# Optimization experiments

Measured on AMD Instinct MI355X. Metric: run time of the kernel, lower is better.

Reference implementation:

```python
import jax, jax.numpy as jnp
import numpy as np

N = 131072   # atoms
D = 384      # aev dim
E = 4        # experts (elements)
H1, H2, H3 = 256, 192, 160


def setup_inputs() -> dict:
    key = jax.random.key(0)
    ks = jax.random.split(key, 12)
    s = 0.05
    inp = {
        "aev": jax.random.normal(ks[0], (N, D), dtype=jnp.float32),
        "index": jax.random.randint(ks[1], (N,), 0, E),
        # stacked per-expert MLP weights [E, in, out]
        "W1": jax.random.normal(ks[2], (E, D, H1), dtype=jnp.float32) * s,
        "b1": jax.random.normal(ks[3], (E, H1), dtype=jnp.float32) * s,
        "W2": jax.random.normal(ks[4], (E, H1, H2), dtype=jnp.float32) * s,
        "b2": jax.random.normal(ks[5], (E, H2), dtype=jnp.float32) * s,
        "W3": jax.random.normal(ks[6], (E, H2, H3), dtype=jnp.float32) * s,
        "b3": jax.random.normal(ks[7], (E, H3), dtype=jnp.float32) * s,
        "W4": jax.random.normal(ks[8], (E, H3, 1), dtype=jnp.float32) * s,
        "b4": jax.random.normal(ks[9], (E, 1), dtype=jnp.float32) * s,
        "alphas": jnp.ones((E,), dtype=jnp.float32),
        "shifts": jnp.array([-0.5, -37.8, -54.5, -75.0], dtype=jnp.float32),
    }
    return inp


def reference(aev, index, W1, b1, W2, b2, W3, b3, W4, b4, alphas, shifts):
    # Run all E expert MLPs densely on all atoms, then select per-atom by index.
    # Same math per selected expert as torch masked dispatch/combine.
    h = jax.nn.celu(jnp.einsum('nd,edh->enh', aev, W1) + b1[:, None, :])
    h = jax.nn.celu(jnp.einsum('enh,ehk->enk', h, W2) + b2[:, None, :])
    h = jax.nn.celu(jnp.einsum('enk,ekm->enm', h, W3) + b3[:, None, :])
    y = (jnp.einsum('enm,emo->eno', h, W4) + b4[:, None, :])[..., 0]  # [E, N]
    y = y * alphas[:, None] + shifts[:, None]                         # shifted nets
    out = jnp.take_along_axis(y, index[None, :], axis=0)[0]           # [N]
    return out
```

## Files before the change

kernel.cpp:

```cpp
#include <hip/hip_runtime.h>
#include <hip/hip_bf16.h>

#define NATOMS 131072
#define DIM    384
#define NE     4
#define H1N    256
#define H2N    192
#define H3N    160
#define BM     64
#define NTH    256
#define NTILES (NATOMS/BM + NE)

typedef __attribute__((ext_vector_type(8))) short bf16x8;
typedef __attribute__((ext_vector_type(4))) float f32x4;
typedef __attribute__((ext_vector_type(4))) int   i32x4;
typedef __attribute__((ext_vector_type(2))) int   i32x2;

#define WS_META   0
#define WS_TABLE  64
#define WS_PERM   (WS_TABLE + NTILES*16)
#define WS_WT1    ((WS_PERM + NATOMS*4 + 255) & ~255)
#define SZ_WT1    (NE*H1N*DIM*2)
#define WS_WT2    (WS_WT1 + SZ_WT1)
#define SZ_WT2    (NE*H2N*H1N*2)
#define WS_WT3    (WS_WT2 + SZ_WT2)
#define SZ_WT3    (NE*H3N*H2N*2)

#define L_ROWS 0
#define L_H1   256
#define L_H2   (L_H1 + BM*528)
#define LDS_TOTAL (L_H2 + BM*400)

static __device__ __forceinline__ unsigned short f2bf(float f) {
  union { __hip_bfloat16 h; unsigned short u; } v;
  v.h = __float2bfloat16(f);
  return v.u;
}
static __device__ __forceinline__ unsigned pack2(float a, float b) {
  union { __hip_bfloat162 h2; unsigned u; } v;
  v.h2 = __float22bfloat162_rn(make_float2(a, b));
  return v.u;
}
static __device__ __forceinline__ float celu1(float x) {
  return x > 0.f ? x : (__expf(x) - 1.f);
}
static __device__ __forceinline__ bf16x8 cvt8(f32x4 a, f32x4 b) {
  union { bf16x8 v; unsigned u[4]; } r;
  r.u[0] = pack2(a.x, a.y); r.u[1] = pack2(a.z, a.w);
  r.u[2] = pack2(b.x, b.y); r.u[3] = pack2(b.z, b.w);
  return r.v;
}

__global__ void k_zero(int* meta) {
  if (threadIdx.x < 16) meta[threadIdx.x] = 0;
}

__global__ void k_wprep(const float* __restrict__ W1, const float* __restrict__ W2,
                        const float* __restrict__ W3,
                        unsigned short* __restrict__ wt1,
                        unsigned short* __restrict__ wt2,
                        unsigned short* __restrict__ wt3) {
  __shared__ float t[32][33];
  int b = blockIdx.x;
  const float* W; unsigned short* wt; int K, NN, ntiles, idx;
  if (b < 384)      { W = W1; wt = wt1; K = 384; NN = 256; ntiles = 8; idx = b; }
  else if (b < 576) { W = W2; wt = wt2; K = 256; NN = 192; ntiles = 6; idx = b - 384; }
  else              { W = W3; wt = wt3; K = 192; NN = 160; ntiles = 5; idx = b - 576; }
  int per_e = (K / 32) * ntiles;
  int e  = idx / per_e;
  int r  = idx % per_e;
  int kt = r / ntiles, nt = r % ntiles;

  int row = threadIdx.x >> 3, c4 = (threadIdx.x & 7) * 4;
  float4 v = *(const float4*)(W + ((size_t)(e * K + kt * 32 + row) * NN + nt * 32 + c4));
  t[row][c4 + 0] = v.x; t[row][c4 + 1] = v.y;
  t[row][c4 + 2] = v.z; t[row][c4 + 3] = v.w;
  __syncthreads();

  int n = threadIdx.x >> 3, k4 = (threadIdx.x & 7) * 4;
  unsigned short o[4];
  o[0] = f2bf(t[k4 + 0][n]); o[1] = f2bf(t[k4 + 1][n]);
  o[2] = f2bf(t[k4 + 2][n]); o[3] = f2bf(t[k4 + 3][n]);
  i32x2 p; p.x = (int)(o[0] | ((unsigned)o[1] << 16));
  p.y = (int)(o[2] | ((unsigned)o[3] << 16));
  *(i32x2*)(wt + ((size_t)(e * (K / 32) + kt) * NN + nt * 32 + n) * 32 + k4) = p;
}

__global__ void k_hist(const int* __restrict__ index, int* __restrict__ meta) {
  __shared__ int h[NE];
  int t = threadIdx.x;
  if (t < NE) h[t] = 0;
  __syncthreads();
  int b0 = blockIdx.x * 1024;
  #pragma unroll
  for (int j = 0; j < 4; ++j) atomicAdd(&h[index[b0 + t + j*256]], 1);
  __syncthreads();
  if (t < NE) atomicAdd(&meta[t], h[t]);
}

__global__ void k_plan(int* __restrict__ meta, i32x4* __restrict__ table) {
  __shared__ int off[NE + 1], nt[NE + 1];
  if (threadIdx.x == 0) {
    int o = 0, t = 0;
    for (int e = 0; e < NE; ++e) {
      off[e] = o; nt[e] = t;
      o += meta[e];
      t += (meta[e] + BM - 1) / BM;
      meta[4 + e] = off[e];
    }
    off[NE] = o; nt[NE] = t;
  }
  __syncthreads();
  for (int i = threadIdx.x; i < NTILES; i += blockDim.x) {
    i32x4 v = {0, 0, 0, 0};
    for (int e = 0; e < NE; ++e) {
      if (i >= nt[e] && i < nt[e + 1]) {
        int local = i - nt[e];
        int cnt = off[e + 1] - off[e];
        int rem = cnt - local * BM;
        v.x = e; v.y = off[e] + local * BM; v.z = rem < BM ? rem : BM;
      }
    }
    table[i] = v;
  }
}

__global__ void k_scatter(const int* __restrict__ index, int* __restrict__ meta,
                          int* __restrict__ perm) {
  __shared__ int h[NE], base[NE];
  int t = threadIdx.x;
  if (t < NE) h[t] = 0;
  __syncthreads();
  int b0 = blockIdx.x * 1024;
  int eIdx[4];
  #pragma unroll
  for (int j = 0; j < 4; ++j) {
    eIdx[j] = index[b0 + t + j*256];
    atomicAdd(&h[eIdx[j]], 1);
  }
  __syncthreads();
  if (t < NE) { base[t] = atomicAdd(&meta[4 + t], h[t]); h[t] = 0; }
  __syncthreads();
  #pragma unroll
  for (int j = 0; j < 4; ++j) {
    int e = eIdx[j];
    int slot = atomicAdd(&h[e], 1);
    perm[base[e] + slot] = b0 + t + j*256;
  }
}

__launch_bounds__(NTH, 2)
__global__ void k_mlp(const float* __restrict__ aev,
                      const unsigned short* __restrict__ wt1,
                      const unsigned short* __restrict__ wt2,
                      const unsigned short* __restrict__ wt3,
                      const float* __restrict__ b1g,
                      const float* __restrict__ b2g,
                      const float* __restrict__ b3g,
                      const float* __restrict__ w4g,
                      const float* __restrict__ b4g,
                      const float* __restrict__ alpg,
                      const float* __restrict__ shfg,
                      const int* __restrict__ perm,
                      const i32x4* __restrict__ table,
                      float* __restrict__ out)
{
  extern __shared__ char smem[];
  int* ldsRows = (int*)(smem + L_ROWS);

  i32x4 tt = table[blockIdx.x];
  const int e = tt.x, start = tt.y, len = tt.z;
  if (len == 0) return;

  const int tid = threadIdx.x;
  const int l   = tid & 63;
  const int w   = tid >> 6;
  const int l15 = l & 15;
  const int lg  = l >> 4;
  const int l4o = lg * 16;
  const int r4  = lg * 4;
  const int wn  = w & 1;
  const int wm  = w >> 1;

  if (tid < BM) ldsRows[tid] = (tid < len) ? perm[start + tid] : -1;

  const float* xp[2];
  #pragma unroll
  for (int mi = 0; mi < 2; ++mi) {
    int row = wm * 32 + mi * 16 + l15;
    int ar = (row < len) ? perm[start + row] : 0;
    xp[mi] = aev + (size_t)ar * DIM + lg * 8;
  }

  {
    f32x4 acc[8][2];
    #pragma unroll
    for (int a = 0; a < 8; ++a)
      #pragma unroll
      for (int b = 0; b < 2; ++b)
        acc[a][b] = f32x4{0.f, 0.f, 0.f, 0.f};

    const unsigned short* w1base =
        wt1 + (size_t)e * (12 * 256 * 32) + (wn * 128 + l15) * 32 + lg * 8;

    bf16x8 af[2][8];
    f32x4  xr[3][2][2];
    #pragma unroll
    for (int s = 0; s < 3; ++s)
      #pragma unroll
      for (int mi = 0; mi < 2; ++mi) {
        xr[s][mi][0] = *(const f32x4*)(xp[mi] + s * 32);
        xr[s][mi][1] = *(const f32x4*)(xp[mi] + s * 32 + 4);
      }
    #pragma unroll
    for (int ni = 0; ni < 8; ++ni)
      af[0][ni] = *(const bf16x8*)(w1base + ni * 512);

    #pragma unroll
    for (int kk = 0; kk < 12; ++kk) {
      const int cb = kk & 1, xb = kk % 3;
      if (kk + 1 < 12) {
        #pragma unroll
        for (int ni = 0; ni < 8; ++ni)
          af[cb ^ 1][ni] = *(const bf16x8*)(w1base + (kk + 1) * 8192 + ni * 512);
      }
      bf16x8 bx[2];
      #pragma unroll
      for (int mi = 0; mi < 2; ++mi) {
        bx[mi] = cvt8(xr[xb][mi][0], xr[xb][mi][1]);
        if (kk + 3 < 12) {
          xr[xb][mi][0] = *(const f32x4*)(xp[mi] + (kk + 3) * 32);
          xr[xb][mi][1] = *(const f32x4*)(xp[mi] + (kk + 3) * 32 + 4);
        }
      }
      #pragma unroll
      for (int ni = 0; ni < 8; ++ni)
        #pragma unroll
        for (int mi = 0; mi < 2; ++mi)
          acc[ni][mi] = __builtin_amdgcn_mfma_f32_16x16x32_bf16(
              af[cb][ni], bx[mi], acc[ni][mi], 0, 0, 0);
    }
    #pragma unroll
    for (int ni = 0; ni < 8; ++ni) {
      const int nb = wn * 128 + ni * 16 + r4;
      float4 bias = *(const float4*)(b1g + e * H1N + nb);
      #pragma unroll
      for (int mi = 0; mi < 2; ++mi) {
        const int m = wm * 32 + mi * 16 + l15;
        f32x4 v = acc[ni][mi];
        i32x2 p;
        p.x = (int)pack2(celu1(v.x + bias.x), celu1(v.y + bias.y));
        p.y = (int)pack2(celu1(v.z + bias.z), celu1(v.w + bias.w));
        *(i32x2*)(smem + L_H1 + m * 528 + nb * 2) = p;
      }
    }
  }
  __syncthreads();

  {
    f32x4 acc[6][2];
    #pragma unroll
    for (int a = 0; a < 6; ++a)
      #pragma unroll
      for (int b = 0; b < 2; ++b)
        acc[a][b] = f32x4{0.f, 0.f, 0.f, 0.f};

    const unsigned short* w2base =
        wt2 + (size_t)e * (8 * 192 * 32) + (wn * 96 + l15) * 32 + lg * 8;
    const int hbase = L_H1 + (wm * 32 + l15) * 528 + l4o;

    bf16x8 af[2][6];
    #pragma unroll
    for (int ni = 0; ni < 6; ++ni)
      af[0][ni] = *(const bf16x8*)(w2base + ni * 512);

    #pragma unroll
    for (int kk = 0; kk < 8; ++kk) {
      const int cb = kk & 1;
      if (kk + 1 < 8) {
        #pragma unroll
        for (int ni = 0; ni < 6; ++ni)
          af[cb ^ 1][ni] = *(const bf16x8*)(w2base + (kk + 1) * 6144 + ni * 512);
      }
      bf16x8 bxh[2];
      #pragma unroll
      for (int mi = 0; mi < 2; ++mi)
        bxh[mi] = *(const bf16x8*)(smem + hbase + mi * 16 * 528 + kk * 64);
      #pragma unroll
      for (int ni = 0; ni < 6; ++ni)
        #pragma unroll
        for (int mi = 0; mi < 2; ++mi)
          acc[ni][mi] = __builtin_amdgcn_mfma_f32_16x16x32_bf16(
              af[cb][ni], bxh[mi], acc[ni][mi], 0, 0, 0);
    }
    #pragma unroll
    for (int ni = 0; ni < 6; ++ni) {
      const int nb = wn * 96 + ni * 16 + r4;
      float4 bias = *(const float4*)(b2g + e * H2N + nb);
      #pragma unroll
      for (int mi = 0; mi < 2; ++mi) {
        const int m = wm * 32 + mi * 16 + l15;
        f32x4 v = acc[ni][mi];
        i32x2 p;
        p.x = (int)pack2(celu1(v.x + bias.x), celu1(v.y + bias.y));
        p.y = (int)pack2(celu1(v.z + bias.z), celu1(v.w + bias.w));
        *(i32x2*)(smem + L_H2 + m * 400 + nb * 2) = p;
      }
    }
  }
  __syncthreads();

  {
    f32x4 acc[5][2];
    #pragma unroll
    for (int a = 0; a < 5; ++a)
      #pragma unroll
      for (int b = 0; b < 2; ++b)
        acc[a][b] = f32x4{0.f, 0.f, 0.f, 0.f};

    const unsigned short* w3base =
        wt3 + (size_t)e * (6 * 160 * 32) + (wn * 80 + l15) * 32 + lg * 8;
    const int hbase = L_H2 + (wm * 32 + l15) * 400 + l4o;

    bf16x8 af[2][5];
    #pragma unroll
    for (int ni = 0; ni < 5; ++ni)
      af[0][ni] = *(const bf16x8*)(w3base + ni * 512);

    #pragma unroll
    for (int kk = 0; kk < 6; ++kk) {
      const int cb = kk & 1;
      if (kk + 1 < 6) {
        #pragma unroll
        for (int ni = 0; ni < 5; ++ni)
          af[cb ^ 1][ni] = *(const bf16x8*)(w3base + (kk + 1) * 5120 + ni * 512);
      }
      bf16x8 bxh[2];
      #pragma unroll
      for (int mi = 0; mi < 2; ++mi)
        bxh[mi] = *(const bf16x8*)(smem + hbase + mi * 16 * 400 + kk * 64);
      #pragma unroll
      for (int ni = 0; ni < 5; ++ni)
        #pragma unroll
        for (int mi = 0; mi < 2; ++mi)
          acc[ni][mi] = __builtin_amdgcn_mfma_f32_16x16x32_bf16(
              af[cb][ni], bxh[mi], acc[ni][mi], 0, 0, 0);
    }
    #pragma unroll
    for (int ni = 0; ni < 5; ++ni) {
      const int nb = wn * 80 + ni * 16 + r4;
      float4 bias = *(const float4*)(b3g + e * H3N + nb);
      #pragma unroll
      for (int mi = 0; mi < 2; ++mi) {
        const int m = wm * 32 + mi * 16 + l15;
        f32x4 v = acc[ni][mi];
        i32x2 p;
        p.x = (int)pack2(celu1(v.x + bias.x), celu1(v.y + bias.y));
        p.y = (int)pack2(celu1(v.z + bias.z), celu1(v.w + bias.w));
        *(i32x2*)(smem + L_H1 + m * 336 + nb * 2) = p;
      }
    }
  }
  __syncthreads();

  {
    const int m = tid >> 2, sub = tid & 3;
    const char* hp = smem + L_H1 + m * 336 + sub * 80;
    const float* wp = w4g + e * H3N + sub * 40;
    float s = 0.f;
    #pragma unroll
    for (int j = 0; j < 5; ++j) {
      i32x4 hv = *(const i32x4*)(hp + j * 16);
      float4 w0 = *(const float4*)(wp + j * 8);
      float4 w1 = *(const float4*)(wp + j * 8 + 4);
      s += __uint_as_float(((unsigned)hv.x) << 16) * w0.x;
      s += __uint_as_float(((unsigned)hv.x) & 0xffff0000u) * w0.y;
      s += __uint_as_float(((unsigned)hv.y) << 16) * w0.z;
      s += __uint_as_float(((unsigned)hv.y) & 0xffff0000u) * w0.w;
      s += __uint_as_float(((unsigned)hv.z) << 16) * w1.x;
      s += __uint_as_float(((unsigned)hv.z) & 0xffff0000u) * w1.y;
      s += __uint_as_float(((unsigned)hv.w) << 16) * w1.z;
      s += __uint_as_float(((unsigned)hv.w) & 0xffff0000u) * w1.w;
    }
    s += __shfl_xor(s, 1);
    s += __shfl_xor(s, 2);
    if (sub == 0 && m < len) {
      float y = (s + b4g[e]) * alpg[e] + shfg[e];
      out[ldsRows[m]] = y;
    }
  }
}

extern "C" void kernel_launch(void* const* d_in, const int* in_sizes, int n_in,
                              void* d_out, int out_size, void* d_ws, size_t ws_size,
                              hipStream_t stream) {
  (void)in_sizes; (void)n_in; (void)out_size; (void)ws_size;
  const float* aev    = (const float*)d_in[0];
  const int*   index  = (const int*)d_in[1];
  const float* W1     = (const float*)d_in[2];
  const float* b1     = (const float*)d_in[3];
  const float* W2     = (const float*)d_in[4];
  const float* b2     = (const float*)d_in[5];
  const float* W3     = (const float*)d_in[6];
  const float* b3     = (const float*)d_in[7];
  const float* W4     = (const float*)d_in[8];
  const float* b4     = (const float*)d_in[9];
  const float* alphas = (const float*)d_in[10];
  const float* shifts = (const float*)d_in[11];
  float* out = (float*)d_out;
  char* ws = (char*)d_ws;

  int*   meta  = (int*)(ws + WS_META);
  i32x4* table = (i32x4*)(ws + WS_TABLE);
  int*   perm  = (int*)(ws + WS_PERM);
  unsigned short* wt1 = (unsigned short*)(ws + WS_WT1);
  unsigned short* wt2 = (unsigned short*)(ws + WS_WT2);
  unsigned short* wt3 = (unsigned short*)(ws + WS_WT3);

  k_zero<<<1, 64, 0, stream>>>(meta);
  k_wprep<<<696, 256, 0, stream>>>(W1, W2, W3, wt1, wt2, wt3);
  k_hist<<<NATOMS/1024, 256, 0, stream>>>(index, meta);
  k_plan<<<1, 256, 0, stream>>>(meta, table);
  k_scatter<<<NATOMS/1024, 256, 0, stream>>>(index, meta, perm);
  k_mlp<<<NTILES, NTH, LDS_TOTAL, stream>>>(
      aev, wt1, wt2, wt3, b1, b2, b3, W4, b4, alphas, shifts, perm, table, out);
}
```

Before: 443.5 us.

## Halve MLP tile rows, hand-schedule global loads with explicit waitcnt pipelining

```diff
diff --git a/kernel.cpp b/kernel.cpp
--- a/kernel.cpp
+++ b/kernel.cpp
@@ -7,7 +7,7 @@
 #define H1N    256
 #define H2N    192
 #define H3N    160
-#define BM     64
+#define BM     32
 #define NTH    256
 #define NTILES (NATOMS/BM + NE)
 
@@ -26,11 +26,6 @@
 #define WS_WT3    (WS_WT2 + SZ_WT2)
 #define SZ_WT3    (NE*H3N*H2N*2)
 
-#define L_ROWS 0
-#define L_H1   256
-#define L_H2   (L_H1 + BM*528)
-#define LDS_TOTAL (L_H2 + BM*400)
-
 static __device__ __forceinline__ unsigned short f2bf(float f) {
   union { __hip_bfloat16 h; unsigned short u; } v;
   v.h = __float2bfloat16(f);
@@ -49,6 +44,19 @@
   r.u[0] = pack2(a.x, a.y); r.u[1] = pack2(a.z, a.w);
   r.u[2] = pack2(b.x, b.y); r.u[3] = pack2(b.z, b.w);
   return r.v;
+}
+
+#define GL16(dst, base, off) \
+  asm volatile("global_load_dwordx4 %0, %1, off offset:%2" \
+               : "=v"(dst) : "v"(base), "n"(off))
+
+template <int N> __device__ __forceinline__ void vmwait() {
+  asm volatile("s_waitcnt vmcnt(%0)" :: "n"(N) : "memory");
+  __builtin_amdgcn_sched_barrier(0);
+}
+static __device__ __forceinline__ void lgkm0_barrier() {
+  asm volatile("s_waitcnt lgkmcnt(0)" ::: "memory");
+  __builtin_amdgcn_s_barrier();
 }
 
 __global__ void k_zero(int* meta) {
@@ -149,7 +157,7 @@
   }
 }
 
-__launch_bounds__(NTH, 2)
+__launch_bounds__(NTH, 3)
 __global__ void k_mlp(const float* __restrict__ aev,
                       const unsigned short* __restrict__ wt1,
                       const unsigned short* __restrict__ wt2,
@@ -165,8 +173,7 @@
                       const i32x4* __restrict__ table,
                       float* __restrict__ out)
 {
-  extern __shared__ char smem[];
-  int* ldsRows = (int*)(smem + L_ROWS);
+  __shared__ char smem[BM * 528];
 
   i32x4 tt = table[blockIdx.x];
   const int e = tt.x, start = tt.y, len = tt.z;
@@ -182,190 +189,209 @@
   const int wn  = w & 1;
   const int wm  = w >> 1;
 
-  if (tid < BM) ldsRows[tid] = (tid < len) ? perm[start + tid] : -1;
-
-  const float* xp[2];
-  #pragma unroll
-  for (int mi = 0; mi < 2; ++mi) {
-    int row = wm * 32 + mi * 16 + l15;
-    int ar = (row < len) ? perm[start + row] : 0;
-    xp[mi] = aev + (size_t)ar * DIM + lg * 8;
-  }
-
+  const int xrow = wm * 16 + l15;
+  const int ar = (xrow < len) ? perm[start + xrow] : 0;
+  const char* xb = (const char*)(aev + (size_t)ar * DIM + lg * 8);
+
+  f32x4 acc[8];
+  bf16x8 ag[2][6];
   {
-    f32x4 acc[8][2];
-    #pragma unroll
-    for (int a = 0; a < 8; ++a)
-      #pragma unroll
-      for (int b = 0; b < 2; ++b)
-        acc[a][b] = f32x4{0.f, 0.f, 0.f, 0.f};
-
-    const unsigned short* w1base =
-        wt1 + (size_t)e * (12 * 256 * 32) + (wn * 128 + l15) * 32 + lg * 8;
-
+    #pragma unroll
+    for (int a = 0; a < 8; ++a) acc[a] = f32x4{0.f, 0.f, 0.f, 0.f};
+
+    const char* wb = (const char*)(wt1 + (size_t)e * (12 * 256 * 32)
+                                   + (size_t)(wn * 128 + l15) * 32 + lg * 8);
+    const char* wb2 = wb + 4096;
     bf16x8 af[2][8];
-    f32x4  xr[3][2][2];
-    #pragma unroll
-    for (int s = 0; s < 3; ++s)
-      #pragma unroll
-      for (int mi = 0; mi < 2; ++mi) {
-        xr[s][mi][0] = *(const f32x4*)(xp[mi] + s * 32);
-        xr[s][mi][1] = *(const f32x4*)(xp[mi] + s * 32 + 4);
-      }
-    #pragma unroll
-    for (int ni = 0; ni < 8; ++ni)
-      af[0][ni] = *(const bf16x8*)(w1base + ni * 512);
-
-    #pragma unroll
-    for (int kk = 0; kk < 12; ++kk) {
-      const int cb = kk & 1, xb = kk % 3;
-      if (kk + 1 < 12) {
-        #pragma unroll
-        for (int ni = 0; ni < 8; ++ni)
-          af[cb ^ 1][ni] = *(const bf16x8*)(w1base + (kk + 1) * 8192 + ni * 512);
-      }
-      bf16x8 bx[2];
-      #pragma unroll
-      for (int mi = 0; mi < 2; ++mi) {
-        bx[mi] = cvt8(xr[xb][mi][0], xr[xb][mi][1]);
-        if (kk + 3 < 12) {
-          xr[xb][mi][0] = *(const f32x4*)(xp[mi] + (kk + 3) * 32);
-          xr[xb][mi][1] = *(const f32x4*)(xp[mi] + (kk + 3) * 32 + 4);
-        }
-      }
-      #pragma unroll
-      for (int ni = 0; ni < 8; ++ni)
-        #pragma unroll
-        for (int mi = 0; mi < 2; ++mi)
-          acc[ni][mi] = __builtin_amdgcn_mfma_f32_16x16x32_bf16(
-              af[cb][ni], bx[mi], acc[ni][mi], 0, 0, 0);
-    }
+    f32x4  xq[3][2];
+
+    GL16(af[0][0], wb, 0);    GL16(af[0][1], wb, 1024);
+    GL16(af[0][2], wb, 2048); GL16(af[0][3], wb, 3072);
+    GL16(af[0][4], wb2, 0);   GL16(af[0][5], wb2, 1024);
+    GL16(af[0][6], wb2, 2048);GL16(af[0][7], wb2, 3072);
+    wb += 16384; wb2 += 16384;
+    GL16(xq[0][0], xb, 0);    GL16(xq[0][1], xb, 16);
+    GL16(xq[1][0], xb, 128);  GL16(xq[1][1], xb, 144);
+    GL16(xq[2][0], xb, 256);  GL16(xq[2][1], xb, 272);
+    xb += 384;
+
+#define L1S(CUR, NXT, QU, NW, PW, PX)                                         \
+  {                                                                           \
+    if (PW) {                                                                 \
+      GL16(af[NXT][0], wb, 0);    GL16(af[NXT][1], wb, 1024);                 \
+      GL16(af[NXT][2], wb, 2048); GL16(af[NXT][3], wb, 3072);                 \
+      GL16(af[NXT][4], wb2, 0);   GL16(af[NXT][5], wb2, 1024);                \
+      GL16(af[NXT][6], wb2, 2048);GL16(af[NXT][7], wb2, 3072);                \
+      wb += 16384; wb2 += 16384;                                              \
+    }                                                                         \
+    vmwait<NW>();                                                             \
+    bf16x8 bx = cvt8(xq[QU][0], xq[QU][1]);                                   \
+    if (PX) { GL16(xq[QU][0], xb, 0); GL16(xq[QU][1], xb, 16); xb += 128; }   \
+    acc[0] = __builtin_amdgcn_mfma_f32_16x16x32_bf16(af[CUR][0], bx, acc[0], 0,0,0); \
+    acc[1] = __builtin_amdgcn_mfma_f32_16x16x32_bf16(af[CUR][1], bx, acc[1], 0,0,0); \
+    acc[2] = __builtin_amdgcn_mfma_f32_16x16x32_bf16(af[CUR][2], bx, acc[2], 0,0,0); \
+    acc[3] = __builtin_amdgcn_mfma_f32_16x16x32_bf16(af[CUR][3], bx, acc[3], 0,0,0); \
+    acc[4] = __builtin_amdgcn_mfma_f32_16x16x32_bf16(af[CUR][4], bx, acc[4], 0,0,0); \
+    acc[5] = __builtin_amdgcn_mfma_f32_16x16x32_bf16(af[CUR][5], bx, acc[5], 0,0,0); \
+    acc[6] = __builtin_amdgcn_mfma_f32_16x16x32_bf16(af[CUR][6], bx, acc[6], 0,0,0); \
+    acc[7] = __builtin_amdgcn_mfma_f32_16x16x32_bf16(af[CUR][7], bx, acc[7], 0,0,0); \
+  }
+
+    L1S(0,1,0,10,1,1)
+    L1S(1,0,1,10,1,1)
+    L1S(0,1,2,10,1,1)
+    L1S(1,0,0,10,1,1)
+    L1S(0,1,1,10,1,1)
+    L1S(1,0,2,10,1,1)
+    L1S(0,1,0,10,1,1)
+    L1S(1,0,1,10,1,1)
+    L1S(0,1,2,10,1,1)
+    L1S(1,0,0,10,1,0)
+    L1S(0,1,1, 8,1,0)
+    L1S(1,0,2, 0,0,0)
+#undef L1S
+
+    const char* wc = (const char*)(wt2 + (size_t)e * (8 * 192 * 32)
+                                   + (size_t)(wn * 96 + l15) * 32 + lg * 8);
+    const char* wc2 = wc + 4096;
+    GL16(ag[0][0], wc, 0);    GL16(ag[0][1], wc, 1024);
+    GL16(ag[0][2], wc, 2048); GL16(ag[0][3], wc, 3072);
+    GL16(ag[0][4], wc2, 0);   GL16(ag[0][5], wc2, 1024);
+    wc += 12288; wc2 += 12288;
+
     #pragma unroll
     for (int ni = 0; ni < 8; ++ni) {
       const int nb = wn * 128 + ni * 16 + r4;
       float4 bias = *(const float4*)(b1g + e * H1N + nb);
+      const int m = wm * 16 + l15;
+      f32x4 v = acc[ni];
+      i32x2 p;
+      p.x = (int)pack2(celu1(v.x + bias.x), celu1(v.y + bias.y));
+      p.y = (int)pack2(celu1(v.z + bias.z), celu1(v.w + bias.w));
+      *(i32x2*)(smem + m * 528 + nb * 2) = p;
+    }
+    lgkm0_barrier();
+
+    f32x4 acc2[6];
+    #pragma unroll
+    for (int a = 0; a < 6; ++a) acc2[a] = f32x4{0.f, 0.f, 0.f, 0.f};
+
+    bf16x8 bxh[8];
+    {
+      const char* hb = smem + (wm * 16 + l15) * 528 + l4o;
       #pragma unroll
-      for (int mi = 0; mi < 2; ++mi) {
-        const int m = wm * 32 + mi * 16 + l15;
-        f32x4 v = acc[ni][mi];
-        i32x2 p;
-        p.x = (int)pack2(celu1(v.x + bias.x), celu1(v.y + bias.y));
-        p.y = (int)pack2(celu1(v.z + bias.z), celu1(v.w + bias.w));
-        *(i32x2*)(smem + L_H1 + m * 528 + nb * 2) = p;
-      }
-    }
-  }
-  __syncthreads();
-
-  {
-    f32x4 acc[6][2];
-    #pragma unroll
-    for (int a = 0; a < 6; ++a)
-      #pragma unroll
-      for (int b = 0; b < 2; ++b)
-        acc[a][b] = f32x4{0.f, 0.f, 0.f, 0.f};
-
-    const unsigned short* w2base =
-        wt2 + (size_t)e * (8 * 192 * 32) + (wn * 96 + l15) * 32 + lg * 8;
-    const int hbase = L_H1 + (wm * 32 + l15) * 528 + l4o;
-
-    bf16x8 af[2][6];
-    #pragma unroll
-    for (int ni = 0; ni < 6; ++ni)
-      af[0][ni] = *(const bf16x8*)(w2base + ni * 512);
-
-    #pragma unroll
-    for (int kk = 0; kk < 8; ++kk) {
-      const int cb = kk & 1;
-      if (kk + 1 < 8) {
-        #pragma unroll
-        for (int ni = 0; ni < 6; ++ni)
-          af[cb ^ 1][ni] = *(const bf16x8*)(w2base + (kk + 1) * 6144 + ni * 512);
-      }
-      bf16x8 bxh[2];
-      #pragma unroll
-      for (int mi = 0; mi < 2; ++mi)
-        bxh[mi] = *(const bf16x8*)(smem + hbase + mi * 16 * 528 + kk * 64);
-      #pragma unroll
-      for (int ni = 0; ni < 6; ++ni)
-        #pragma unroll
-        for (int mi = 0; mi < 2; ++mi)
-          acc[ni][mi] = __builtin_amdgcn_mfma_f32_16x16x32_bf16(
-              af[cb][ni], bxh[mi], acc[ni][mi], 0, 0, 0);
-    }
+      for (int kk = 0; kk < 8; ++kk)
+        bxh[kk] = *(const bf16x8*)(hb + kk * 64);
+    }
+    asm volatile("s_waitcnt lgkmcnt(0)" ::: "memory");
+    __builtin_amdgcn_sched_barrier(0);
+    __builtin_amdgcn_s_barrier();
+
+#define L2S(CUR, NXT, KK, NW, PW)                                             \
+  {                                                                           \
+    if (PW) {                                                                 \
+      GL16(ag[NXT][0], wc, 0);    GL16(ag[NXT][1], wc, 1024);                 \
+      GL16(ag[NXT][2], wc, 2048); GL16(ag[NXT][3], wc, 3072);                 \
+      GL16(ag[NXT][4], wc2, 0);   GL16(ag[NXT][5], wc2, 1024);                \
+      wc += 12288; wc2 += 12288;                                              \
+    }                                                                         \
+    vmwait<NW>();                                                             \
+    acc2[0] = __builtin_amdgcn_mfma_f32_16x16x32_bf16(ag[CUR][0], bxh[KK], acc2[0], 0,0,0); \
+    acc2[1] = __builtin_amdgcn_mfma_f32_16x16x32_bf16(ag[CUR][1], bxh[KK], acc2[1], 0,0,0); \
+    acc2[2] = __builtin_amdgcn_mfma_f32_16x16x32_bf16(ag[CUR][2], bxh[KK], acc2[2], 0,0,0); \
+    acc2[3] = __builtin_amdgcn_mfma_f32_16x16x32_bf16(ag[CUR][3], bxh[KK], acc2[3], 0,0,0); \
+    acc2[4] = __builtin_amdgcn_mfma_f32_16x16x32_bf16(ag[CUR][4], bxh[KK], acc2[4], 0,0,0); \
+    acc2[5] = __builtin_amdgcn_mfma_f32_16x16x32_bf16(ag[CUR][5], bxh[KK], acc2[5], 0,0,0); \
+  }
+
+    L2S(0,1,0,6,1)
+    L2S(1,0,1,6,1)
+    L2S(0,1,2,6,1)
+    L2S(1,0,3,6,1)
+    L2S(0,1,4,6,1)
+    L2S(1,0,5,6,1)
+    L2S(0,1,6,6,1)
+    L2S(1,0,7,0,0)
+#undef L2S
+
+    const char* wd = (const char*)(wt3 + (size_t)e * (6 * 160 * 32)
+                                   + (size_t)(wn * 80 + l15) * 32 + lg * 8);
+    const char* wd2 = wd + 4096;
+    bf16x8 ah[2][5];
+    GL16(ah[0][0], wd, 0);    GL16(ah[0][1], wd, 1024);
+    GL16(ah[0][2], wd, 2048); GL16(ah[0][3], wd, 3072);
+    GL16(ah[0][4], wd2, 0);
+    wd += 10240; wd2 += 10240;
+
     #pragma unroll
     for (int ni = 0; ni < 6; ++ni) {
       const int nb = wn * 96 + ni * 16 + r4;
       float4 bias = *(const float4*)(b2g + e * H2N + nb);
+      const int m = wm * 16 + l15;
+      f32x4 v = acc2[ni];
+      i32x2 p;
+      p.x = (int)pack2(celu1(v.x + bias.x), celu1(v.y + bias.y));
+      p.y = (int)pack2(celu1(v.z + bias.z), celu1(v.w + bias.w));
+      *(i32x2*)(smem + m * 400 + nb * 2) = p;
+    }
+    lgkm0_barrier();
+
+    f32x4 acc3[5];
+    #pragma unroll
+    for (int a = 0; a < 5; ++a) acc3[a] = f32x4{0.f, 0.f, 0.f, 0.f};
+
+    bf16x8 bxi[6];
+    {
+      const char* hb = smem + (wm * 16 + l15) * 400 + l4o;
       #pragma unroll
-      for (int mi = 0; mi < 2; ++mi) {
-        const int m = wm * 32 + mi * 16 + l15;
-        f32x4 v = acc[ni][mi];
-        i32x2 p;
-        p.x = (int)pack2(celu1(v.x + bias.x), celu1(v.y + bias.y));
-        p.y = (int)pack2(celu1(v.z + bias.z), celu1(v.w + bias.w));
-        *(i32x2*)(smem + L_H2 + m * 400 + nb * 2) = p;
-      }
-    }
-  }
-  __syncthreads();
-
-  {
-    f32x4 acc[5][2];
-    #pragma unroll
-    for (int a = 0; a < 5; ++a)
-      #pragma unroll
-      for (int b = 0; b < 2; ++b)
-        acc[a][b] = f32x4{0.f, 0.f, 0.f, 0.f};
-
-    const unsigned short* w3base =
-        wt3 + (size_t)e * (6 * 160 * 32) + (wn * 80 + l15) * 32 + lg * 8;
-    const int hbase = L_H2 + (wm * 32 + l15) * 400 + l4o;
-
-    bf16x8 af[2][5];
-    #pragma unroll
-    for (int ni = 0; ni < 5; ++ni)
-      af[0][ni] = *(const bf16x8*)(w3base + ni * 512);
-
-    #pragma unroll
-    for (int kk = 0; kk < 6; ++kk) {
-      const int cb = kk & 1;
-      if (kk + 1 < 6) {
-        #pragma unroll
-        for (int ni = 0; ni < 5; ++ni)
-          af[cb ^ 1][ni] = *(const bf16x8*)(w3base + (kk + 1) * 5120 + ni * 512);
-      }
-      bf16x8 bxh[2];
-      #pragma unroll
-      for (int mi = 0; mi < 2; ++mi)
-        bxh[mi] = *(const bf16x8*)(smem + hbase + mi * 16 * 400 + kk * 64);
-      #pragma unroll
-      for (int ni = 0; ni < 5; ++ni)
-        #pragma unroll
-        for (int mi = 0; mi < 2; ++mi)
-          acc[ni][mi] = __builtin_amdgcn_mfma_f32_16x16x32_bf16(
-              af[cb][ni], bxh[mi], acc[ni][mi], 0, 0, 0);
-    }
+      for (int kk = 0; kk < 6; ++kk)
+        bxi[kk] = *(const bf16x8*)(hb + kk * 64);
+    }
+    asm volatile("s_waitcnt lgkmcnt(0)" ::: "memory");
+    __builtin_amdgcn_sched_barrier(0);
+    __builtin_amdgcn_s_barrier();
+
+#define L3S(CUR, NXT, KK, NW, PW)                                             \
+  {                                                                           \
+    if (PW) {                                                                 \
+      GL16(ah[NXT][0], wd, 0);    GL16(ah[NXT][1], wd, 1024);                 \
+      GL16(ah[NXT][2], wd, 2048); GL16(ah[NXT][3], wd, 3072);                 \
+      GL16(ah[NXT][4], wd2, 0);                                               \
+      wd += 10240; wd2 += 10240;                                              \
+    }                                                                         \
+    vmwait<NW>();                                                             \
+    acc3[0] = __builtin_amdgcn_mfma_f32_16x16x32_bf16(ah[CUR][0], bxi[KK], acc3[0], 0,0,0); \
+    acc3[1] = __builtin_amdgcn_mfma_f32_16x16x32_bf16(ah[CUR][1], bxi[KK], acc3[1], 0,0,0); \
+    acc3[2] = __builtin_amdgcn_mfma_f32_16x16x32_bf16(ah[CUR][2], bxi[KK], acc3[2], 0,0,0); \
+    acc3[3] = __builtin_amdgcn_mfma_f32_16x16x32_bf16(ah[CUR][3], bxi[KK], acc3[3], 0,0,0); \
+    acc3[4] = __builtin_amdgcn_mfma_f32_16x16x32_bf16(ah[CUR][4], bxi[KK], acc3[4], 0,0,0); \
+  }
+
+    L3S(0,1,0,5,1)
+    L3S(1,0,1,5,1)
+    L3S(0,1,2,5,1)
+    L3S(1,0,3,5,1)
+    L3S(0,1,4,5,1)
+    L3S(1,0,5,0,0)
+#undef L3S
+
     #pragma unroll
     for (int ni = 0; ni < 5; ++ni) {
       const int nb = wn * 80 + ni * 16 + r4;
       float4 bias = *(const float4*)(b3g + e * H3N + nb);
-      #pragma unroll
-      for (int mi = 0; mi < 2; ++mi) {
-        const int m = wm * 32 + mi * 16 + l15;
-        f32x4 v = acc[ni][mi];
-        i32x2 p;
-        p.x = (int)pack2(celu1(v.x + bias.x), celu1(v.y + bias.y));
-        p.y = (int)pack2(celu1(v.z + bias.z), celu1(v.w + bias.w));
-        *(i32x2*)(smem + L_H1 + m * 336 + nb * 2) = p;
-      }
-    }
-  }
-  __syncthreads();
-
-  {
+      const int m = wm * 16 + l15;
+      f32x4 v = acc3[ni];
+      i32x2 p;
+      p.x = (int)pack2(celu1(v.x + bias.x), celu1(v.y + bias.y));
+      p.y = (int)pack2(celu1(v.z + bias.z), celu1(v.w + bias.w));
+      *(i32x2*)(smem + m * 336 + nb * 2) = p;
+    }
+    lgkm0_barrier();
+  }
+
+  if (tid < 4 * BM) {
     const int m = tid >> 2, sub = tid & 3;
-    const char* hp = smem + L_H1 + m * 336 + sub * 80;
+    const char* hp = smem + m * 336 + sub * 80;
     const float* wp = w4g + e * H3N + sub * 40;
     float s = 0.f;
     #pragma unroll
@@ -386,7 +412,7 @@
     s += __shfl_xor(s, 2);
     if (sub == 0 && m < len) {
       float y = (s + b4g[e]) * alpg[e] + shfg[e];
-      out[ldsRows[m]] = y;
+      out[perm[start + m]] = y;
     }
   }
 }
@@ -422,6 +448,6 @@
   k_hist<<<NATOMS/1024, 256, 0, stream>>>(index, meta);
   k_plan<<<1, 256, 0, stream>>>(meta, table);
   k_scatter<<<NATOMS/1024, 256, 0, stream>>>(index, meta, perm);
-  k_mlp<<<NTILES, NTH, LDS_TOTAL, stream>>>(
+  k_mlp<<<NTILES, NTH, 0, stream>>>(
       aev, wt1, wt2, wt3, b1, b2, b3, W4, b4, alphas, shifts, perm, table, out);
 }
```

Result: slower. 475.2 us (+7.1%).

## Stage expert weights into LDS via async global_load_lds double buffering

Applied to the files above, without the earlier changes.

```diff
diff --git a/kernel.cpp b/kernel.cpp
--- a/kernel.cpp
+++ b/kernel.cpp
@@ -24,12 +24,11 @@
 #define WS_WT2    (WS_WT1 + SZ_WT1)
 #define SZ_WT2    (NE*H2N*H1N*2)
 #define WS_WT3    (WS_WT2 + SZ_WT2)
-#define SZ_WT3    (NE*H3N*H2N*2)
-
-#define L_ROWS 0
-#define L_H1   256
-#define L_H2   (L_H1 + BM*528)
-#define LDS_TOTAL (L_H2 + BM*400)
+#define SZ_WT3    (NE*H3N*H2N*2 + 4096)
+
+#define L_SLOT(i) ((i)*16384)
+#define L_H       32768
+#define LDS_TOTAL (L_H + BM*528)
 
 static __device__ __forceinline__ unsigned short f2bf(float f) {
   union { __hip_bfloat16 h; unsigned short u; } v;
@@ -50,6 +49,15 @@
   r.u[2] = pack2(b.x, b.y); r.u[3] = pack2(b.z, b.w);
   return r.v;
 }
+
+#define SCHEDB __builtin_amdgcn_sched_barrier(0)
+#define VMWAIT(N) do { asm volatile("s_waitcnt vmcnt(" #N ")" ::: "memory"); SCHEDB; } while(0)
+#define LGKM0  do { asm volatile("s_waitcnt lgkmcnt(0)" ::: "memory"); SCHEDB; } while(0)
+#define BARRIER do { __builtin_amdgcn_s_barrier(); SCHEDB; } while(0)
+
+#define GLDS16(gp, lp) __builtin_amdgcn_global_load_lds( \
+    (const __attribute__((address_space(1))) unsigned int*)(gp), \
+    (__attribute__((address_space(3))) unsigned int*)(lp), 16, 0, 0)
 
 __global__ void k_zero(int* meta) {
   if (threadIdx.x < 16) meta[threadIdx.x] = 0;
@@ -166,7 +174,6 @@
                       float* __restrict__ out)
 {
   extern __shared__ char smem[];
-  int* ldsRows = (int*)(smem + L_ROWS);
 
   i32x4 tt = table[blockIdx.x];
   const int e = tt.x, start = tt.y, len = tt.z;
@@ -177,218 +184,215 @@
   const int w   = tid >> 6;
   const int l15 = l & 15;
   const int lg  = l >> 4;
-  const int l4o = lg * 16;
-  const int r4  = lg * 4;
-  const int wn  = w & 1;
-  const int wm  = w >> 1;
-
-  if (tid < BM) ldsRows[tid] = (tid < len) ? perm[start + tid] : -1;
-
-  const float* xp[2];
-  #pragma unroll
-  for (int mi = 0; mi < 2; ++mi) {
-    int row = wm * 32 + mi * 16 + l15;
-    int ar = (row < len) ? perm[start + row] : 0;
-    xp[mi] = aev + (size_t)ar * DIM + lg * 8;
-  }
-
-  {
-    f32x4 acc[8][2];
-    #pragma unroll
-    for (int a = 0; a < 8; ++a)
-      #pragma unroll
-      for (int b = 0; b < 2; ++b)
-        acc[a][b] = f32x4{0.f, 0.f, 0.f, 0.f};
-
-    const unsigned short* w1base =
-        wt1 + (size_t)e * (12 * 256 * 32) + (wn * 128 + l15) * 32 + lg * 8;
-
-    bf16x8 af[2][8];
-    f32x4  xr[3][2][2];
-    #pragma unroll
-    for (int s = 0; s < 3; ++s)
-      #pragma unroll
-      for (int mi = 0; mi < 2; ++mi) {
-        xr[s][mi][0] = *(const f32x4*)(xp[mi] + s * 32);
-        xr[s][mi][1] = *(const f32x4*)(xp[mi] + s * 32 + 4);
+
+  const char* w1c = (const char*)wt1 + (size_t)e * (12 * 16384);
+  const char* w2c = (const char*)wt2 + (size_t)e * (8 * 12288);
+  const char* w3c = (const char*)wt3 + (size_t)e * (6 * 10240);
+
+#define STAGE4(GB, SLOT) do { \
+    const char* _g = (GB) + w * 4096 + l * 16; \
+    char* _l = smem + L_SLOT(SLOT) + w * 4096; \
+    GLDS16(_g, _l); GLDS16(_g + 1024, _l + 1024); \
+    GLDS16(_g + 2048, _l + 2048); GLDS16(_g + 3072, _l + 3072); \
+    SCHEDB; \
+  } while (0)
+#define STAGE3(GB, SLOT) do { \
+    const char* _g = (GB) + w * 3072 + l * 16; \
+    char* _l = smem + L_SLOT(SLOT) + w * 3072; \
+    GLDS16(_g, _l); GLDS16(_g + 1024, _l + 1024); GLDS16(_g + 2048, _l + 2048); \
+    SCHEDB; \
+  } while (0)
+
+  const float* xp[4];
+  #pragma unroll
+  for (int mf = 0; mf < 4; ++mf) {
+    int r = mf * 16 + l15;
+    int ar = (r < len) ? perm[start + r] : 0;
+    xp[mf] = aev + (size_t)ar * DIM + lg * 8;
+  }
+
+  STAGE4(w1c, 0);
+  f32x4 xq[2][4][2];
+  #pragma unroll
+  for (int s = 0; s < 2; ++s)
+    #pragma unroll
+    for (int mf = 0; mf < 4; ++mf) {
+      xq[s][mf][0] = *(const f32x4*)(xp[mf] + s * 32);
+      xq[s][mf][1] = *(const f32x4*)(xp[mf] + s * 32 + 4);
+    }
+  SCHEDB;
+
+  f32x4 acc[4][4];
+  #pragma unroll
+  for (int a = 0; a < 4; ++a)
+    #pragma unroll
+    for (int b = 0; b < 4; ++b)
+      acc[a][b] = f32x4{0.f, 0.f, 0.f, 0.f};
+  float4 b1v[4];
+
+  #pragma unroll
+  for (int kk = 0; kk < 12; ++kk) {
+    if (kk < 11) VMWAIT(8); else VMWAIT(0);
+    BARRIER;
+    if (kk == 11) {
+      #pragma unroll
+      for (int ni = 0; ni < 4; ++ni)
+        b1v[ni] = *(const float4*)(b1g + e * H1N + w * 64 + ni * 16 + lg * 4);
+      SCHEDB;
+    }
+    if (kk < 11) STAGE4(w1c + (kk + 1) * 16384, (kk + 1) & 1);
+    else         STAGE3(w2c, 0);
+    bf16x8 bx[4];
+    #pragma unroll
+    for (int mf = 0; mf < 4; ++mf)
+      bx[mf] = cvt8(xq[kk & 1][mf][0], xq[kk & 1][mf][1]);
+    if (kk < 10) {
+      #pragma unroll
+      for (int mf = 0; mf < 4; ++mf) {
+        xq[kk & 1][mf][0] = *(const f32x4*)(xp[mf] + (kk + 2) * 32);
+        xq[kk & 1][mf][1] = *(const f32x4*)(xp[mf] + (kk + 2) * 32 + 4);
       }
-    #pragma unroll
-    for (int ni = 0; ni < 8; ++ni)
-      af[0][ni] = *(const bf16x8*)(w1base + ni * 512);
-
-    #pragma unroll
-    for (int kk = 0; kk < 12; ++kk) {
-      const int cb = kk & 1, xb = kk % 3;
-      if (kk + 1 < 12) {
+      SCHEDB;
+    }
+    #pragma unroll
+    for (int ni = 0; ni < 4; ++ni) {
+      bf16x8 af = *(const bf16x8*)(smem + L_SLOT(kk & 1)
+                                   + (w * 64 + ni * 16 + l15) * 64 + lg * 16);
+      #pragma unroll
+      for (int mf = 0; mf < 4; ++mf)
+        acc[ni][mf] = __builtin_amdgcn_mfma_f32_16x16x32_bf16(
+            af, bx[mf], acc[ni][mf], 0, 0, 0);
+    }
+  }
+
+  #pragma unroll
+  for (int ni = 0; ni < 4; ++ni) {
+    const int nb = w * 64 + ni * 16 + lg * 4;
+    #pragma unroll
+    for (int mf = 0; mf < 4; ++mf) {
+      f32x4 v = acc[ni][mf];
+      i32x2 p;
+      p.x = (int)pack2(celu1(v.x + b1v[ni].x), celu1(v.y + b1v[ni].y));
+      p.y = (int)pack2(celu1(v.z + b1v[ni].z), celu1(v.w + b1v[ni].w));
+      *(i32x2*)(smem + L_H + (mf * 16 + l15) * 528 + nb * 2) = p;
+    }
+  }
+  LGKM0; BARRIER;
+
+  f32x4 acc2[3][4];
+  #pragma unroll
+  for (int a = 0; a < 3; ++a)
+    #pragma unroll
+    for (int b = 0; b < 4; ++b)
+      acc2[a][b] = f32x4{0.f, 0.f, 0.f, 0.f};
+  float4 b2v[3];
+
+  #pragma unroll
+  for (int c = 0; c < 8; ++c) {
+    VMWAIT(0);
+    BARRIER;
+    if (c == 7) {
+      #pragma unroll
+      for (int ni = 0; ni < 3; ++ni)
+        b2v[ni] = *(const float4*)(b2g + e * H2N + w * 48 + ni * 16 + lg * 4);
+      SCHEDB;
+    }
+    if (c < 7) STAGE3(w2c + (c + 1) * 12288, (c + 1) & 1);
+    else       STAGE3(w3c, 0);
+    bf16x8 bh[4];
+    #pragma unroll
+    for (int mf = 0; mf < 4; ++mf)
+      bh[mf] = *(const bf16x8*)(smem + L_H + (mf * 16 + l15) * 528 + c * 64 + lg * 16);
+    #pragma unroll
+    for (int ni = 0; ni < 3; ++ni) {
+      bf16x8 af = *(const bf16x8*)(smem + L_SLOT(c & 1)
+                                   + (w * 48 + ni * 16 + l15) * 64 + lg * 16);
+      #pragma unroll
+      for (int mf = 0; mf < 4; ++mf)
+        acc2[ni][mf] = __builtin_amdgcn_mfma_f32_16x16x32_bf16(
+            af, bh[mf], acc2[ni][mf], 0, 0, 0);
+    }
+  }
+
+  BARRIER;
+  #pragma unroll
+  for (int ni = 0; ni < 3; ++ni) {
+    const int nb = w * 48 + ni * 16 + lg * 4;
+    #pragma unroll
+    for (int mf = 0; mf < 4; ++mf) {
+      f32x4 v = acc2[ni][mf];
+      i32x2 p;
+      p.x = (int)pack2(celu1(v.x + b2v[ni].x), celu1(v.y + b2v[ni].y));
+      p.y = (int)pack2(celu1(v.z + b2v[ni].z), celu1(v.w + b2v[ni].w));
+      *(i32x2*)(smem + L_H + (mf * 16 + l15) * 400 + nb * 2) = p;
+    }
+  }
+  LGKM0; BARRIER;
+
+  const int nf3 = (w < 2) ? 3 : 2;
+  f32x4 acc3[3][4];
+  #pragma unroll
+  for (int a = 0; a < 3; ++a)
+    #pragma unroll
+    for (int b = 0; b < 4; ++b)
+      acc3[a][b] = f32x4{0.f, 0.f, 0.f, 0.f};
+
+  #pragma unroll
+  for (int u = 0; u < 6; ++u) {
+    VMWAIT(0);
+    BARRIER;
+    if (u < 5) STAGE3(w3c + (u + 1) * 10240, (u + 1) & 1);
+    bf16x8 bh[4];
+    #pragma unroll
+    for (int mf = 0; mf < 4; ++mf)
+      bh[mf] = *(const bf16x8*)(smem + L_H + (mf * 16 + l15) * 400 + u * 64 + lg * 16);
+    #pragma unroll
+    for (int ni = 0; ni < 3; ++ni) {
+      if (ni < nf3) {
+        bf16x8 af = *(const bf16x8*)(smem + L_SLOT(u & 1)
+                                     + ((w + ni * 4) * 16 + l15) * 64 + lg * 16);
         #pragma unroll
-        for (int ni = 0; ni < 8; ++ni)
-          af[cb ^ 1][ni] = *(const bf16x8*)(w1base + (kk + 1) * 8192 + ni * 512);
+        for (int mf = 0; mf < 4; ++mf)
+          acc3[ni][mf] = __builtin_amdgcn_mfma_f32_16x16x32_bf16(
+              af, bh[mf], acc3[ni][mf], 0, 0, 0);
       }
-      bf16x8 bx[2];
-      #pragma unroll
-      for (int mi = 0; mi < 2; ++mi) {
-        bx[mi] = cvt8(xr[xb][mi][0], xr[xb][mi][1]);
-        if (kk + 3 < 12) {
-          xr[xb][mi][0] = *(const f32x4*)(xp[mi] + (kk + 3) * 32);
-          xr[xb][mi][1] = *(const f32x4*)(xp[mi] + (kk + 3) * 32 + 4);
-        }
+    }
+  }
+
+  BARRIER;
+  float part[4] = {0.f, 0.f, 0.f, 0.f};
+  #pragma unroll
+  for (int ni = 0; ni < 3; ++ni) {
+    if (ni < nf3) {
+      const int nb = (w + ni * 4) * 16 + lg * 4;
+      float4 b3v = *(const float4*)(b3g + e * H3N + nb);
+      float4 w4v = *(const float4*)(w4g + e * H3N + nb);
+      #pragma unroll
+      for (int mf = 0; mf < 4; ++mf) {
+        f32x4 v = acc3[ni][mf];
+        part[mf] += celu1(v.x + b3v.x) * w4v.x + celu1(v.y + b3v.y) * w4v.y
+                  + celu1(v.z + b3v.z) * w4v.z + celu1(v.w + b3v.w) * w4v.w;
       }
-      #pragma unroll
-      for (int ni = 0; ni < 8; ++ni)
-        #pragma unroll
-        for (int mi = 0; mi < 2; ++mi)
-          acc[ni][mi] = __builtin_amdgcn_mfma_f32_16x16x32_bf16(
-              af[cb][ni], bx[mi], acc[ni][mi], 0, 0, 0);
-    }
-    #pragma unroll
-    for (int ni = 0; ni < 8; ++ni) {
-      const int nb = wn * 128 + ni * 16 + r4;
-      float4 bias = *(const float4*)(b1g + e * H1N + nb);
-      #pragma unroll
-      for (int mi = 0; mi < 2; ++mi) {
-        const int m = wm * 32 + mi * 16 + l15;
-        f32x4 v = acc[ni][mi];
-        i32x2 p;
-        p.x = (int)pack2(celu1(v.x + bias.x), celu1(v.y + bias.y));
-        p.y = (int)pack2(celu1(v.z + bias.z), celu1(v.w + bias.w));
-        *(i32x2*)(smem + L_H1 + m * 528 + nb * 2) = p;
-      }
-    }
-  }
-  __syncthreads();
-
-  {
-    f32x4 acc[6][2];
-    #pragma unroll
-    for (int a = 0; a < 6; ++a)
-      #pragma unroll
-      for (int b = 0; b < 2; ++b)
-        acc[a][b] = f32x4{0.f, 0.f, 0.f, 0.f};
-
-    const unsigned short* w2base =
-        wt2 + (size_t)e * (8 * 192 * 32) + (wn * 96 + l15) * 32 + lg * 8;
-    const int hbase = L_H1 + (wm * 32 + l15) * 528 + l4o;
-
-    bf16x8 af[2][6];
-    #pragma unroll
-    for (int ni = 0; ni < 6; ++ni)
-      af[0][ni] = *(const bf16x8*)(w2base + ni * 512);
-
-    #pragma unroll
-    for (int kk = 0; kk < 8; ++kk) {
-      const int cb = kk & 1;
-      if (kk + 1 < 8) {
-        #pragma unroll
-        for (int ni = 0; ni < 6; ++ni)
-          af[cb ^ 1][ni] = *(const bf16x8*)(w2base + (kk + 1) * 6144 + ni * 512);
-      }
-      bf16x8 bxh[2];
-      #pragma unroll
-      for (int mi = 0; mi < 2; ++mi)
-        bxh[mi] = *(const bf16x8*)(smem + hbase + mi * 16 * 528 + kk * 64);
-      #pragma unroll
-      for (int ni = 0; ni < 6; ++ni)
-        #pragma unroll
-        for (int mi = 0; mi < 2; ++mi)
-          acc[ni][mi] = __builtin_amdgcn_mfma_f32_16x16x32_bf16(
-              af[cb][ni], bxh[mi], acc[ni][mi], 0, 0, 0);
-    }
-    #pragma unroll
-    for (int ni = 0; ni < 6; ++ni) {
-      const int nb = wn * 96 + ni * 16 + r4;
-      float4 bias = *(const float4*)(b2g + e * H2N + nb);
-      #pragma unroll
-      for (int mi = 0; mi < 2; ++mi) {
-        const int m = wm * 32 + mi * 16 + l15;
-        f32x4 v = acc[ni][mi];
-        i32x2 p;
-        p.x = (int)pack2(celu1(v.x + bias.x), celu1(v.y + bias.y));
-        p.y = (int)pack2(celu1(v.z + bias.z), celu1(v.w + bias.w));
-        *(i32x2*)(smem + L_H2 + m * 400 + nb * 2) = p;
-      }
-    }
-  }
-  __syncthreads();
-
-  {
-    f32x4 acc[5][2];
-    #pragma unroll
-    for (int a = 0; a < 5; ++a)
-      #pragma unroll
-      for (int b = 0; b < 2; ++b)
-        acc[a][b] = f32x4{0.f, 0.f, 0.f, 0.f};
-
-    const unsigned short* w3base =
-        wt3 + (size_t)e * (6 * 160 * 32) + (wn * 80 + l15) * 32 + lg * 8;
-    const int hbase = L_H2 + (wm * 32 + l15) * 400 + l4o;
-
-    bf16x8 af[2][5];
-    #pragma unroll
-    for (int ni = 0; ni < 5; ++ni)
-      af[0][ni] = *(const bf16x8*)(w3base + ni * 512);
-
-    #pragma unroll
-    for (int kk = 0; kk < 6; ++kk) {
-      const int cb = kk & 1;
-      if (kk + 1 < 6) {
-        #pragma unroll
-        for (int ni = 0; ni < 5; ++ni)
-          af[cb ^ 1][ni] = *(const bf16x8*)(w3base + (kk + 1) * 5120 + ni * 512);
-      }
-      bf16x8 bxh[2];
-      #pragma unroll
-      for (int mi = 0; mi < 2; ++mi)
-        bxh[mi] = *(const bf16x8*)(smem + hbase + mi * 16 * 400 + kk * 64);
-      #pragma unroll
-      for (int ni = 0; ni < 5; ++ni)
-        #pragma unroll
-        for (int mi = 0; mi < 2; ++mi)
-          acc[ni][mi] = __builtin_amdgcn_mfma_f32_16x16x32_bf16(
-              af[cb][ni], bxh[mi], acc[ni][mi], 0, 0, 0);
-    }
-    #pragma unroll
-    for (int ni = 0; ni < 5; ++ni) {
-      const int nb = wn * 80 + ni * 16 + r4;
-      float4 bias = *(const float4*)(b3g + e * H3N + nb);
-      #pragma unroll
-      for (int mi = 0; mi < 2; ++mi) {
-        const int m = wm * 32 + mi * 16 + l15;
-        f32x4 v = acc[ni][mi];
-        i32x2 p;
-        p.x = (int)pack2(celu1(v.x + bias.x), celu1(v.y + bias.y));
-        p.y = (int)pack2(celu1(v.z + bias.z), celu1(v.w + bias.w));
-        *(i32x2*)(smem + L_H1 + m * 336 + nb * 2) = p;
-      }
-    }
-  }
-  __syncthreads();
-
-  {
-    const int m = tid >> 2, sub = tid & 3;
-    const char* hp = smem + L_H1 + m * 336 + sub * 80;
-    const float* wp = w4g + e * H3N + sub * 40;
-    float s = 0.f;
-    #pragma unroll
-    for (int j = 0; j < 5; ++j) {
-      i32x4 hv = *(const i32x4*)(hp + j * 16);
-      float4 w0 = *(const float4*)(wp + j * 8);
-      float4 w1 = *(const float4*)(wp + j * 8 + 4);
-      s += __uint_as_float(((unsigned)hv.x) << 16) * w0.x;
-      s += __uint_as_float(((unsigned)hv.x) & 0xffff0000u) * w0.y;
-      s += __uint_as_float(((unsigned)hv.y) << 16) * w0.z;
-      s += __uint_as_float(((unsigned)hv.y) & 0xffff0000u) * w0.w;
-      s += __uint_as_float(((unsigned)hv.z) << 16) * w1.x;
-      s += __uint_as_float(((unsigned)hv.z) & 0xffff0000u) * w1.y;
-      s += __uint_as_float(((unsigned)hv.w) << 16) * w1.z;
-      s += __uint_as_float(((unsigned)hv.w) & 0xffff0000u) * w1.w;
-    }
-    s += __shfl_xor(s, 1);
-    s += __shfl_xor(s, 2);
-    if (sub == 0 && m < len) {
-      float y = (s + b4g[e]) * alpg[e] + shfg[e];
-      out[ldsRows[m]] = y;
-    }
-  }
+    }
+  }
+  #pragma unroll
+  for (int mf = 0; mf < 4; ++mf) {
+    part[mf] += __shfl_xor(part[mf], 16);
+    part[mf] += __shfl_xor(part[mf], 32);
+  }
+  float* pb = (float*)smem;
+  if (lg == 0) {
+    #pragma unroll
+    for (int mf = 0; mf < 4; ++mf) pb[w * 64 + mf * 16 + l15] = part[mf];
+  }
+  LGKM0; BARRIER;
+  if (tid < BM && tid < len) {
+    float s = pb[tid] + pb[64 + tid] + pb[128 + tid] + pb[192 + tid];
+    float y = (s + b4g[e]) * alpg[e] + shfg[e];
+    out[perm[start + tid]] = y;
+  }
+#undef STAGE4
+#undef STAGE3
 }
 
 extern "C" void kernel_launch(void* const* d_in, const int* in_sizes, int n_in,
@@ -417,6 +421,9 @@
   unsigned short* wt2 = (unsigned short*)(ws + WS_WT2);
   unsigned short* wt3 = (unsigned short*)(ws + WS_WT3);
 
+  hipFuncSetAttribute((const void*)k_mlp,
+                      hipFuncAttributeMaxDynamicSharedMemorySize, LDS_TOTAL);
+
   k_zero<<<1, 64, 0, stream>>>(meta);
   k_wprep<<<696, 256, 0, stream>>>(W1, W2, W3, wt1, wt2, wt3);
   k_hist<<<NATOMS/1024, 256, 0, stream>>>(index, meta);
```

Measured after the change: 427.8 us. 1.04x faster.
